# Kernel optimization log

Measured on AMD Instinct MI355X. Metric: run time of the kernel, lower is better.

## Reference

```python
import jax, jax.numpy as jnp
import numpy as np

E = 256
H = 8
DH = E // H
N = 200000
NEG = -1e9


def _normalize(x, eps=1e-12):
    # torch F.normalize: x / max(||x||_2, eps) along last dim
    n = jnp.linalg.norm(x, axis=-1, keepdims=True)
    return x / jnp.maximum(n, eps)


def setup_inputs() -> dict:
    key = jax.random.key(0)
    ks = jax.random.split(key, 16)
    s = 1.0 / np.sqrt(E)
    inp = {
        "context_vector": jax.random.normal(ks[0], (3 * E,), jnp.float32),
        "node_embeddings": jax.random.normal(ks[1], (N, E), jnp.float32),
        "invalid_action_mask": jax.random.randint(ks[2], (N,), 0, 2).astype(bool),
        # project_context: Linear(3E, E)
        "Wc": jax.random.normal(ks[3], (E, 3 * E), jnp.float32) * (1.0 / np.sqrt(3 * E)),
        "bc": jnp.zeros((E,), jnp.float32),
        # project_keys / project_values: Linear(E, E)
        "Wk": jax.random.normal(ks[4], (E, E), jnp.float32) * s,
        "bk": jnp.zeros((E,), jnp.float32),
        "Wv": jax.random.normal(ks[5], (E, E), jnp.float32) * s,
        "bv": jnp.zeros((E,), jnp.float32),
        # nn.MultiheadAttention packed in-projection and out-projection
        "in_proj_w": jax.random.normal(ks[6], (3 * E, E), jnp.float32) * s,
        "in_proj_b": jnp.zeros((3 * E,), jnp.float32),
        "out_proj_w": jax.random.normal(ks[7], (E, E), jnp.float32) * s,
        "out_proj_b": jnp.zeros((E,), jnp.float32),
        # project_attn_output: Linear(E, E)
        "Wo": jax.random.normal(ks[8], (E, E), jnp.float32) * s,
        "bo": jnp.zeros((E,), jnp.float32),
    }
    # guarantee at least one valid action
    inp["invalid_action_mask"] = inp["invalid_action_mask"].at[0].set(False)
    return inp


def reference(context_vector, node_embeddings, invalid_action_mask,
              Wc, bc, Wk, bk, Wv, bv,
              in_proj_w, in_proj_b, out_proj_w, out_proj_b, Wo, bo):
    valid = ~invalid_action_mask                        # [N]

    query = context_vector @ Wc.T + bc                  # [E]
    keys = _normalize(node_embeddings @ Wk.T + bk)      # [N, E]
    values = _normalize(node_embeddings @ Wv.T + bv)    # [N, E]

    # MultiheadAttention, single query, batch 1
    wq, wk2, wv2 = in_proj_w[:E], in_proj_w[E:2 * E], in_proj_w[2 * E:]
    bq, bk2, bv2 = in_proj_b[:E], in_proj_b[E:2 * E], in_proj_b[2 * E:]
    q = (query @ wq.T + bq).reshape(H, DH)              # [H, DH]
    k = (keys @ wk2.T + bk2).reshape(N, H, DH)          # [N, H, DH]
    v = (values @ wv2.T + bv2).reshape(N, H, DH)

    logits = jnp.einsum("hd,nhd->hn", q, k) / np.sqrt(DH)   # [H, N]
    logits = jnp.where(valid[None, :], logits, NEG)
    w = jax.nn.softmax(logits, axis=-1)                 # [H, N]
    attn = jnp.einsum("hn,nhd->hd", w, v).reshape(E)    # [E]
    attn = attn @ out_proj_w.T + out_proj_b             # [E]

    attn = _normalize(attn @ Wo.T + bo)                 # [E]

    # pointer scores over valid nodes (invalid -> prob 0)
    scores = jnp.where(valid, keys @ attn, NEG)         # [N]
    probs = jax.nn.softmax(scores)                      # [N]
    return probs
```

## Files before the change

### kernel.cpp

```cpp
#include <hip/hip_runtime.h>

#define NN 200000
#define NEGV -1000000000.0f

typedef __attribute__((ext_vector_type(8))) short bf16x8;
typedef __attribute__((ext_vector_type(4))) float f32x4;
typedef __attribute__((ext_vector_type(4))) unsigned int u32x4;

__device__ __forceinline__ float bf2f(unsigned short u){
  unsigned int x = ((unsigned int)u) << 16;
  return __builtin_bit_cast(float, x);
}
__device__ __forceinline__ unsigned short f2bf(float f){
  unsigned int x = __builtin_bit_cast(unsigned int, f);
  x += 0x7fffu + ((x >> 16) & 1u);
  return (unsigned short)(x >> 16);
}

static constexpr size_t OFF_RK     = 0;
static constexpr size_t OFF_RV     = 800256;
static constexpr size_t OFF_LOGITS = 1600512;
static constexpr size_t OFF_SCORES = 8000512;
static constexpr size_t OFF_QUERY  = 8800768;
static constexpr size_t OFF_Q2     = 8801792;
static constexpr size_t OFF_A2     = 8802816;
static constexpr size_t OFF_CONSTS = 8811008;
static constexpr size_t OFF_BIMG   = 8811264;
static constexpr size_t OFF_LSTAT  = 9081600;
static constexpr size_t OFF_MZ     = 9089792;
static constexpr size_t OFF_KATTN  = 9089856;
static constexpr size_t OFF_KB     = 9090880;
static constexpr size_t OFF_UPART  = 9090944;
static constexpr size_t OFF_TPART  = 13285248;
static constexpr size_t OFF_U      = 13301632;
static constexpr size_t OFF_T      = 13309824;
static constexpr size_t OFF_P3STAT = 13309888;
static constexpr size_t OFF_MZ3    = 13313984;
static constexpr size_t OFF_EMBBF  = 13314048;
static constexpr size_t WS_NEED_BF = OFF_EMBBF + (size_t)NN*512;

__global__ void k_conv(const float* __restrict__ emb, unsigned char* __restrict__ ebf){
  size_t stride = (size_t)gridDim.x * blockDim.x;
  for (size_t g = (size_t)blockIdx.x*blockDim.x + threadIdx.x; g < (size_t)NN*32; g += stride){
    const float* src = emb + g*8;
    float4 a = *(const float4*)src;
    float4 b = *(const float4*)(src + 4);
    u32x4 o;
    o.x = (unsigned int)f2bf(a.x) | ((unsigned int)f2bf(a.y) << 16);
    o.y = (unsigned int)f2bf(a.z) | ((unsigned int)f2bf(a.w) << 16);
    o.z = (unsigned int)f2bf(b.x) | ((unsigned int)f2bf(b.y) << 16);
    o.w = (unsigned int)f2bf(b.z) | ((unsigned int)f2bf(b.w) << 16);
    *(u32x4*)(ebf + g*16) = o;
  }
}

__global__ void k_prep1(const float* __restrict__ ctx, const float* __restrict__ Wc,
                        const float* __restrict__ bc, float* __restrict__ query){
  int tid = threadIdx.x, lane = tid & 63, wave = tid >> 6;
  float4 c0 = *(const float4*)(ctx + lane*4);
  float4 c1 = *(const float4*)(ctx + 256 + lane*4);
  float4 c2 = *(const float4*)(ctx + 512 + lane*4);
  #pragma unroll
  for (int rr = 0; rr < 2; rr++){
    int r = blockIdx.x*8 + wave*2 + rr;
    float4 w0 = *(const float4*)(Wc + (size_t)r*768 + lane*4);
    float4 w1 = *(const float4*)(Wc + (size_t)r*768 + 256 + lane*4);
    float4 w2 = *(const float4*)(Wc + (size_t)r*768 + 512 + lane*4);
    float d = w0.x*c0.x + w0.y*c0.y + w0.z*c0.z + w0.w*c0.w
            + w1.x*c1.x + w1.y*c1.y + w1.z*c1.z + w1.w*c1.w
            + w2.x*c2.x + w2.y*c2.y + w2.z*c2.z + w2.w*c2.w;
    #pragma unroll
    for (int m = 1; m < 64; m <<= 1) d += __shfl_xor(d, m);
    if (lane == 0) query[r] = d + bc[r];
  }
}

__global__ void k_prep2(const float* __restrict__ ipw, const float* __restrict__ ipb,
                        const float* __restrict__ query, float* __restrict__ q2){
  int tid = threadIdx.x, lane = tid & 63, wave = tid >> 6;
  float4 x4 = *(const float4*)(query + lane*4);
  #pragma unroll
  for (int rr = 0; rr < 2; rr++){
    int r = blockIdx.x*8 + wave*2 + rr;
    float4 w4 = *(const float4*)(ipw + (size_t)r*256 + lane*4);
    float d = w4.x*x4.x + w4.y*x4.y + w4.z*x4.z + w4.w*x4.w;
    #pragma unroll
    for (int m = 1; m < 64; m <<= 1) d += __shfl_xor(d, m);
    if (lane == 0) q2[r] = d + ipb[r];
  }
}

__global__ void k_prep3(const float* __restrict__ ipw, const float* __restrict__ ipb,
                        const float* __restrict__ q2, float* __restrict__ AH,
                        float* __restrict__ consts){
  int h = blockIdx.x, t = threadIdx.x;
  __shared__ float qs[32];
  if (t < 32) qs[t] = q2[h*32 + t];
  __syncthreads();
  float a = 0.f;
  #pragma unroll
  for (int d = 0; d < 32; d++) a += qs[d] * ipw[(size_t)(256 + h*32 + d)*256 + t];
  AH[h*256 + t] = a;
  if (t == 0){
    float ck = 0.f;
    for (int d = 0; d < 32; d++) ck += qs[d] * ipb[256 + h*32 + d];
    consts[8 + h] = ck;
  }
}

__global__ void k_prep4(const float* __restrict__ Wk, const float* __restrict__ AH,
                        float* __restrict__ A2p){
  int b = blockIdx.x, h = b >> 3, seg = b & 7, t = threadIdx.x;
  __shared__ float as[32];
  if (t < 32) as[t] = AH[h*256 + seg*32 + t];
  __syncthreads();
  float acc = 0.f;
  #pragma unroll
  for (int i = 0; i < 32; i++) acc += as[i] * Wk[(size_t)(seg*32 + i)*256 + t];
  A2p[(size_t)b*256 + t] = acc;
}

__global__ void k_prep5(const float* __restrict__ A2p, const float* __restrict__ AH,
                        const float* __restrict__ bk, float* __restrict__ A2,
                        float* __restrict__ consts){
  int h = blockIdx.x, t = threadIdx.x, lane = t & 63, wave = t >> 6;
  float s = 0.f;
  #pragma unroll
  for (int seg = 0; seg < 8; seg++) s += A2p[(size_t)(h*8 + seg)*256 + t];
  A2[h*256 + t] = s;
  float cc = AH[h*256 + t] * bk[t];
  #pragma unroll
  for (int m = 1; m < 64; m <<= 1) cc += __shfl_xor(cc, m);
  __shared__ float red[4];
  if (lane == 0) red[wave] = cc;
  __syncthreads();
  if (t == 0) consts[h] = red[0] + red[1] + red[2] + red[3];
}

__global__ void k_bimg(const float* __restrict__ Wk, const float* __restrict__ Wv,
                       const float* __restrict__ A2, unsigned char* __restrict__ bimg){
  int g = blockIdx.x*256 + threadIdx.x;
  if (g >= 8*528*4) return;
  int s = g / (528*4);
  int rem = g % (528*4);
  int col = rem >> 2, kg = rem & 3;
  int j0 = s*32 + kg*8;
  const float* src = nullptr;
  if (col < 256) src = Wk + col*256 + j0;
  else if (col < 512) src = Wv + (col-256)*256 + j0;
  else if (col < 520) src = A2 + (col-512)*256 + j0;
  unsigned short u[8];
  #pragma unroll
  for (int i = 0; i < 8; i++) u[i] = src ? f2bf(src[i]) : (unsigned short)0;
  uint4 o;
  o.x = (unsigned int)u[0] | ((unsigned int)u[1] << 16);
  o.y = (unsigned int)u[2] | ((unsigned int)u[3] << 16);
  o.z = (unsigned int)u[4] | ((unsigned int)u[5] << 16);
  o.w = (unsigned int)u[6] | ((unsigned int)u[7] << 16);
  unsigned int addr = (unsigned int)((col*64 + kg*16) ^ ((col & 7) << 4));
  *(uint4*)(bimg + (size_t)s*33792 + addr) = o;
}

template<int BF>
__launch_bounds__(256)
__global__ void k_main(const float* __restrict__ emb, const unsigned char* __restrict__ ebf,
                       const unsigned char* __restrict__ bimg,
                       const int* __restrict__ mask, const float* __restrict__ consts,
                       float* __restrict__ rk_g, float* __restrict__ rv_g,
                       float* __restrict__ logits){
  __shared__ float part[4][2][16];
  __shared__ float rkbuf[32];
  const int tid = threadIdx.x;
  const int lane = tid & 63, ch = tid >> 6;
  const int c = lane & 15, kg = lane >> 4;
  const int nb0 = blockIdx.x * 32;
  const unsigned bOff = (unsigned)((c*64 + kg*16) ^ ((c & 7) << 4));

  f32x4 acc[2][9];
  #pragma unroll
  for (int st = 0; st < 2; st++)
    #pragma unroll
    for (int f = 0; f < 9; f++) acc[st][f] = (f32x4){0.f, 0.f, 0.f, 0.f};

  if (BF){
    const unsigned char* aB0 = ebf + (size_t)(nb0 + c)*512 + kg*16;
    const unsigned char* aB1 = ebf + (size_t)(nb0 + 16 + c)*512 + kg*16;
    bf16x8 pa0[8], pa1[8];
    pa0[0] = *(const bf16x8*)(aB0);
    pa1[0] = *(const bf16x8*)(aB1);
    pa0[1] = *(const bf16x8*)(aB0 + 64);
    pa1[1] = *(const bf16x8*)(aB1 + 64);
    #pragma unroll
    for (int s = 0; s < 8; s++){
      if (s < 6){
        pa0[s+2] = *(const bf16x8*)(aB0 + (s+2)*64);
        pa1[s+2] = *(const bf16x8*)(aB1 + (s+2)*64);
      }
      const unsigned char* bs = bimg + (size_t)s*33792 + bOff;
      #pragma unroll
      for (int f = 0; f < 9; f++){
        const int cf = (f < 8) ? (ch*8 + f) : 32;
        bf16x8 bfv = *(const bf16x8*)(bs + (size_t)cf*1024);
        acc[0][f] = __builtin_amdgcn_mfma_f32_16x16x32_bf16(pa0[s], bfv, acc[0][f], 0, 0, 0);
        acc[1][f] = __builtin_amdgcn_mfma_f32_16x16x32_bf16(pa1[s], bfv, acc[1][f], 0, 0, 0);
      }
    }
  } else {
    #pragma unroll 2
    for (int s = 0; s < 8; s++){
      const float* a0p = emb + (size_t)(nb0 + c)*256 + s*32 + kg*8;
      const float* a1p = emb + (size_t)(nb0 + 16 + c)*256 + s*32 + kg*8;
      float4 x0 = *(const float4*)a0p, x1 = *(const float4*)(a0p + 4);
      float4 y0 = *(const float4*)a1p, y1 = *(const float4*)(a1p + 4);
      u32x4 u0, u1;
      u0.x = (unsigned int)f2bf(x0.x) | ((unsigned int)f2bf(x0.y) << 16);
      u0.y = (unsigned int)f2bf(x0.z) | ((unsigned int)f2bf(x0.w) << 16);
      u0.z = (unsigned int)f2bf(x1.x) | ((unsigned int)f2bf(x1.y) << 16);
      u0.w = (unsigned int)f2bf(x1.z) | ((unsigned int)f2bf(x1.w) << 16);
      u1.x = (unsigned int)f2bf(y0.x) | ((unsigned int)f2bf(y0.y) << 16);
      u1.y = (unsigned int)f2bf(y0.z) | ((unsigned int)f2bf(y0.w) << 16);
      u1.z = (unsigned int)f2bf(y1.x) | ((unsigned int)f2bf(y1.y) << 16);
      u1.w = (unsigned int)f2bf(y1.z) | ((unsigned int)f2bf(y1.w) << 16);
      bf16x8 af0 = __builtin_bit_cast(bf16x8, u0);
      bf16x8 af1 = __builtin_bit_cast(bf16x8, u1);
      const unsigned char* bs = bimg + (size_t)s*33792 + bOff;
      #pragma unroll
      for (int f = 0; f < 9; f++){
        const int cf = (f < 8) ? (ch*8 + f) : 32;
        bf16x8 bfv = *(const bf16x8*)(bs + (size_t)cf*1024);
        acc[0][f] = __builtin_amdgcn_mfma_f32_16x16x32_bf16(af0, bfv, acc[0][f], 0, 0, 0);
        acc[1][f] = __builtin_amdgcn_mfma_f32_16x16x32_bf16(af1, bfv, acc[1][f], 0, 0, 0);
      }
    }
  }

  #pragma unroll
  for (int st = 0; st < 2; st++){
    #pragma unroll
    for (int i = 0; i < 4; i++){
      float pp = 0.f;
      #pragma unroll
      for (int f = 0; f < 8; f++) pp += acc[st][f][i]*acc[st][f][i];
      #pragma unroll
      for (int m = 1; m < 16; m <<= 1) pp += __shfl_xor(pp, m);
      if (c == 0) part[ch][st][kg*4 + i] = pp;
    }
  }
  __syncthreads();
  if (tid < 32){
    int gs = tid >> 4, r = tid & 15;
    float rk = fmaxf(sqrtf(part[0][gs][r] + part[1][gs][r]), 1e-12f);
    float rv = fmaxf(sqrtf(part[2][gs][r] + part[3][gs][r]), 1e-12f);
    rk_g[nb0 + tid] = rk; rv_g[nb0 + tid] = rv;
    rkbuf[tid] = rk;
  }
  __syncthreads();
  if (ch == 3 && c < 8){
    const float rs32 = 0.17677669529663688f;
    float cb = consts[c], ck = consts[8 + c];
    #pragma unroll
    for (int st = 0; st < 2; st++){
      #pragma unroll
      for (int i = 0; i < 4; i++){
        int nl = st*16 + kg*4 + i;
        int n = nb0 + nl;
        float lg = (mask[n] == 0) ? ((acc[st][8][i] + cb)*rs32/rkbuf[nl] + ck*rs32) : NEGV;
        logits[(size_t)n*8 + c] = lg;
      }
    }
  }
}

__global__ void k_lstats(const float* __restrict__ logits, float* __restrict__ lstat){
  int tid = threadIdx.x;
  float m[8], z[8];
  #pragma unroll
  for (int h = 0; h < 8; h++){ m[h] = -3.0e38f; z[h] = 0.f; }
  for (int n = blockIdx.x*256 + tid; n < NN; n += 128*256){
    float4 a = *(const float4*)(logits + (size_t)n*8);
    float4 b = *(const float4*)(logits + (size_t)n*8 + 4);
    float l[8] = {a.x,a.y,a.z,a.w,b.x,b.y,b.z,b.w};
    #pragma unroll
    for (int h = 0; h < 8; h++){
      float M = fmaxf(m[h], l[h]);
      z[h] = z[h]*expf(m[h]-M) + expf(l[h]-M);
      m[h] = M;
    }
  }
  #pragma unroll
  for (int s = 1; s < 64; s <<= 1){
    #pragma unroll
    for (int h = 0; h < 8; h++){
      float m2 = __shfl_xor(m[h], s), z2 = __shfl_xor(z[h], s);
      float M = fmaxf(m[h], m2);
      z[h] = z[h]*expf(m[h]-M) + z2*expf(m2-M);
      m[h] = M;
    }
  }
  __shared__ float sm[4][8], sz[4][8];
  int wave = tid >> 6, lane = tid & 63;
  if (lane == 0){
    #pragma unroll
    for (int h = 0; h < 8; h++){ sm[wave][h] = m[h]; sz[wave][h] = z[h]; }
  }
  __syncthreads();
  if (tid < 8){
    float M = sm[0][tid], Z = sz[0][tid];
    #pragma unroll
    for (int w = 1; w < 4; w++){
      float M2 = fmaxf(M, sm[w][tid]);
      Z = Z*expf(M-M2) + sz[w][tid]*expf(sm[w][tid]-M2);
      M = M2;
    }
    lstat[(blockIdx.x*8 + tid)*2] = M;
    lstat[(blockIdx.x*8 + tid)*2 + 1] = Z;
  }
}

__global__ void k_mz(const float* __restrict__ lstat, float* __restrict__ MZ){
  int t = threadIdx.x;
  int h = t >> 3, seg = t & 7;
  float m = -3.0e38f, z = 0.f;
  for (int k = 0; k < 16; k++){
    int b = seg*16 + k;
    float m2 = lstat[(b*8 + h)*2], z2 = lstat[(b*8 + h)*2 + 1];
    float M = fmaxf(m, m2); z = z*expf(m-M) + z2*expf(m2-M); m = M;
  }
  #pragma unroll
  for (int s = 1; s < 8; s <<= 1){
    float m2 = __shfl_xor(m, s), z2 = __shfl_xor(z, s);
    float M = fmaxf(m, m2); z = z*expf(m-M) + z2*expf(m2-M); m = M;
  }
  if (seg == 0){ MZ[h] = m; MZ[8+h] = z; }
}

template<int BF>
__launch_bounds__(256)
__global__ void k_wsum(const void* __restrict__ embsrc, const float* __restrict__ logits,
                       const float* __restrict__ rv_g, const float* __restrict__ MZ,
                       float* __restrict__ upart, float* __restrict__ tpart){
  int tid = threadIdx.x, lane = tid & 63, wave = tid >> 6;
  int hl = lane & 31, h2 = lane >> 5;
  int gw = blockIdx.x*4 + wave;
  float Mh = MZ[hl & 7];
  float ua[8][8];
  #pragma unroll
  for (int h = 0; h < 8; h++)
    #pragma unroll
    for (int j = 0; j < 8; j++) ua[h][j] = 0.f;
  float tacc = 0.f;
  for (int p = gw; p < NN/2; p += 2048){
    int n = 2*p + h2;
    float e[8];
    if (BF){
      uint4 g = *(const uint4*)((const unsigned char*)embsrc + (size_t)n*512 + hl*16);
      e[0]=bf2f((unsigned short)(g.x&0xffff)); e[1]=bf2f((unsigned short)(g.x>>16));
      e[2]=bf2f((unsigned short)(g.y&0xffff)); e[3]=bf2f((unsigned short)(g.y>>16));
      e[4]=bf2f((unsigned short)(g.z&0xffff)); e[5]=bf2f((unsigned short)(g.z>>16));
      e[6]=bf2f((unsigned short)(g.w&0xffff)); e[7]=bf2f((unsigned short)(g.w>>16));
    } else {
      const float* ep = (const float*)embsrc + (size_t)n*256 + hl*8;
      float4 a = *(const float4*)ep, b = *(const float4*)(ep + 4);
      e[0]=a.x; e[1]=a.y; e[2]=a.z; e[3]=a.w; e[4]=b.x; e[5]=b.y; e[6]=b.z; e[7]=b.w;
    }
    float coef = 0.f;
    if (hl < 8) coef = expf(logits[(size_t)n*8 + hl] - Mh) / rv_g[n];
    tacc += coef;
    #pragma unroll
    for (int h = 0; h < 8; h++){
      float ch = __shfl(coef, h, 32);
      #pragma unroll
      for (int j = 0; j < 8; j++) ua[h][j] += ch * e[j];
    }
  }
  #pragma unroll
  for (int h = 0; h < 8; h++)
    #pragma unroll
    for (int j = 0; j < 8; j++) ua[h][j] += __shfl_xor(ua[h][j], 32);
  tacc += __shfl_xor(tacc, 32);
  __shared__ float ub[4][8][256];
  __shared__ float tb[4][8];
  if (h2 == 0){
    #pragma unroll
    for (int h = 0; h < 8; h++)
      #pragma unroll
      for (int j = 0; j < 8; j++) ub[wave][h][hl*8 + j] = ua[h][j];
    if (hl < 8) tb[wave][hl] = tacc;
  }
  __syncthreads();
  #pragma unroll
  for (int rep = 0; rep < 8; rep++){
    int idx = rep*256 + tid;
    int h = idx >> 8, j = idx & 255;
    upart[(size_t)blockIdx.x*2048 + h*256 + j] = ub[0][h][j]+ub[1][h][j]+ub[2][h][j]+ub[3][h][j];
  }
  if (tid < 8) tpart[blockIdx.x*8 + tid] = tb[0][tid]+tb[1][tid]+tb[2][tid]+tb[3][tid];
}

__global__ void k_ured(const float* __restrict__ upart, const float* __restrict__ tpart,
                       float* __restrict__ U, float* __restrict__ T){
  int b = blockIdx.x; int h = b >> 3, js = b & 7;
  int t = threadIdx.x; int j = js*32 + (t & 31); int br = t >> 5;
  float s = 0.f;
  for (int k = 0; k < 64; k++){
    int bb = k*8 + br;
    s += upart[(size_t)bb*2048 + h*256 + j];
  }
  __shared__ float sb[8][32];
  sb[br][t & 31] = s;
  __syncthreads();
  if (t < 32){
    float tot = 0.f;
    #pragma unroll
    for (int r = 0; r < 8; r++) tot += sb[r][t];
    U[h*256 + js*32 + t] = tot;
  }
  if (js == 0){
    float tp = 0.f;
    for (int i = t; i < 512; i += 256) tp += tpart[i*8 + h];
    #pragma unroll
    for (int m = 1; m < 64; m <<= 1) tp += __shfl_xor(tp, m);
    __shared__ float rr[4];
    if ((t & 63) == 0) rr[t >> 6] = tp;
    __syncthreads();
    if (t == 0) T[h] = rr[0]+rr[1]+rr[2]+rr[3];
  }
}

__global__ void k_att1(const float* __restrict__ U, const float* __restrict__ T,
                       const float* __restrict__ MZ, const float* __restrict__ Wv,
                       const float* __restrict__ bv, float* __restrict__ sh2g){
  int tid = threadIdx.x, lane = tid & 63, wave = tid >> 6;
  float4 uh[8];
  #pragma unroll
  for (int h = 0; h < 8; h++) uh[h] = *(const float4*)(U + h*256 + lane*4);
  #pragma unroll
  for (int rr = 0; rr < 2; rr++){
    int r = blockIdx.x*8 + wave*2 + rr;
    float4 w4 = *(const float4*)(Wv + (size_t)r*256 + lane*4);
    float acc[8];
    #pragma unroll
    for (int h = 0; h < 8; h++)
      acc[h] = w4.x*uh[h].x + w4.y*uh[h].y + w4.z*uh[h].z + w4.w*uh[h].w;
    #pragma unroll
    for (int m = 1; m < 64; m <<= 1)
      #pragma unroll
      for (int h = 0; h < 8; h++) acc[h] += __shfl_xor(acc[h], m);
    if (lane == 0){
      float bvr = bv[r];
      #pragma unroll
      for (int h = 0; h < 8; h++) sh2g[h*256 + r] = (acc[h] + bvr*T[h]) / MZ[8+h];
    }
  }
}

__global__ void k_att2(const float* __restrict__ ipw, const float* __restrict__ ipb,
                       const float* __restrict__ sh2g, float* __restrict__ a1g){
  int tid = threadIdx.x, lane = tid & 63, wave = tid >> 6;
  #pragma unroll
  for (int rr = 0; rr < 2; rr++){
    int r = blockIdx.x*8 + wave*2 + rr;
    int h = r >> 5;
    float4 x4 = *(const float4*)(sh2g + h*256 + lane*4);
    float4 w4 = *(const float4*)(ipw + (size_t)(512 + r)*256 + lane*4);
    float d = w4.x*x4.x + w4.y*x4.y + w4.z*x4.z + w4.w*x4.w;
    #pragma unroll
    for (int m = 1; m < 64; m <<= 1) d += __shfl_xor(d, m);
    if (lane == 0) a1g[r] = d + ipb[512 + r];
  }
}

__global__ void k_matvec(const float* __restrict__ W, const float* __restrict__ b,
                         const float* __restrict__ x, float* __restrict__ y){
  int tid = threadIdx.x, lane = tid & 63, wave = tid >> 6;
  float4 x4 = *(const float4*)(x + lane*4);
  #pragma unroll
  for (int rr = 0; rr < 2; rr++){
    int r = blockIdx.x*8 + wave*2 + rr;
    float4 w4 = *(const float4*)(W + (size_t)r*256 + lane*4);
    float d = w4.x*x4.x + w4.y*x4.y + w4.z*x4.z + w4.w*x4.w;
    #pragma unroll
    for (int m = 1; m < 64; m <<= 1) d += __shfl_xor(d, m);
    if (lane == 0) y[r] = d + b[r];
  }
}

__global__ void k_att5(const float* __restrict__ Wk, const float* __restrict__ o2g,
                       float* __restrict__ kp){
  int b = blockIdx.x, t = threadIdx.x;
  __shared__ float os[32];
  if (t < 32) os[t] = o2g[b*32 + t];
  __syncthreads();
  float acc = 0.f;
  #pragma unroll
  for (int i = 0; i < 32; i++) acc += os[i] * Wk[(size_t)(b*32 + i)*256 + t];
  kp[b*256 + t] = acc;
}

__global__ void k_fin(const float* __restrict__ o2g, const float* __restrict__ kp,
                      const float* __restrict__ bk, float* __restrict__ kattn,
                      float* __restrict__ kbout){
  int t = threadIdx.x, lane = t & 63, wave = t >> 6;
  __shared__ float red[4], red2[4];
  float o2v = o2g[t];
  float sq = o2v*o2v;
  #pragma unroll
  for (int m = 1; m < 64; m <<= 1) sq += __shfl_xor(sq, m);
  if (lane == 0) red[wave] = sq;
  float cb = o2v * bk[t];
  #pragma unroll
  for (int m = 1; m < 64; m <<= 1) cb += __shfl_xor(cb, m);
  if (lane == 0) red2[wave] = cb;
  __syncthreads();
  float nrm = fmaxf(sqrtf(red[0]+red[1]+red[2]+red[3]), 1e-12f);
  float s = 0.f;
  #pragma unroll
  for (int b = 0; b < 8; b++) s += kp[b*256 + t];
  kattn[t] = s / nrm;
  if (t == 0) kbout[0] = (red2[0]+red2[1]+red2[2]+red2[3]) / nrm;
}

template<int BF>
__launch_bounds__(256)
__global__ void k_scores(const void* __restrict__ embsrc, const float* __restrict__ rk_g,
                         const int* __restrict__ mask, const float* __restrict__ kattn,
                         const float* __restrict__ kbp, float* __restrict__ scores,
                         float* __restrict__ p3stat){
  int tid = threadIdx.x, lane = tid & 63, wave = tid >> 6;
  int hl = lane & 31, h2 = lane >> 5;
  __shared__ float ka[256];
  ka[tid] = kattn[tid];
  __syncthreads();
  float kb = kbp[0];
  float kv[8];
  #pragma unroll
  for (int j = 0; j < 8; j++) kv[j] = ka[hl*8 + j];
  int gw = blockIdx.x*4 + wave;
  float m = -3.0e38f, z = 0.f;
  for (int p = gw; p < NN/2; p += 2048){
    int n = 2*p + h2;
    float d;
    if (BF){
      uint4 g = *(const uint4*)((const unsigned char*)embsrc + (size_t)n*512 + hl*16);
      d  = bf2f((unsigned short)(g.x&0xffff))*kv[0] + bf2f((unsigned short)(g.x>>16))*kv[1];
      d += bf2f((unsigned short)(g.y&0xffff))*kv[2] + bf2f((unsigned short)(g.y>>16))*kv[3];
      d += bf2f((unsigned short)(g.z&0xffff))*kv[4] + bf2f((unsigned short)(g.z>>16))*kv[5];
      d += bf2f((unsigned short)(g.w&0xffff))*kv[6] + bf2f((unsigned short)(g.w>>16))*kv[7];
    } else {
      const float* ep = (const float*)embsrc + (size_t)n*256 + hl*8;
      float4 a = *(const float4*)ep, b = *(const float4*)(ep + 4);
      d = a.x*kv[0]+a.y*kv[1]+a.z*kv[2]+a.w*kv[3]+b.x*kv[4]+b.y*kv[5]+b.z*kv[6]+b.w*kv[7];
    }
    #pragma unroll
    for (int s = 1; s < 32; s <<= 1) d += __shfl_xor(d, s);
    if (hl == 0){
      float sc = (mask[n] == 0) ? ((d + kb) / rk_g[n]) : NEGV;
      scores[n] = sc;
      float M = fmaxf(m, sc);
      z = z*expf(m - M) + expf(sc - M);
      m = M;
    }
  }
  float m2 = __shfl_xor(m, 32), z2 = __shfl_xor(z, 32);
  float M = fmaxf(m, m2); z = z*expf(m-M) + z2*expf(m2-M); m = M;
  __shared__ float rm[4], rz[4];
  if (lane == 0){ rm[wave] = m; rz[wave] = z; }
  __syncthreads();
  if (tid == 0){
    float Mx = rm[0], Z = rz[0];
    for (int w = 1; w < 4; w++){
      float M2 = fmaxf(Mx, rm[w]);
      Z = Z*expf(Mx - M2) + rz[w]*expf(rm[w] - M2);
      Mx = M2;
    }
    p3stat[blockIdx.x*2] = Mx; p3stat[blockIdx.x*2+1] = Z;
  }
}

__global__ void k_mz3(const float* __restrict__ p3stat, float* __restrict__ MZ3){
  int t = threadIdx.x;
  float m = p3stat[t*2], z = p3stat[t*2+1];
  {
    float m2 = p3stat[(t+256)*2], z2 = p3stat[(t+256)*2+1];
    float M = fmaxf(m, m2); z = z*expf(m-M) + z2*expf(m2-M); m = M;
  }
  #pragma unroll
  for (int mm = 1; mm < 64; mm <<= 1){
    float ms = __shfl_xor(m, mm), zs = __shfl_xor(z, mm);
    float Mx = fmaxf(m, ms); z = z*expf(m-Mx) + zs*expf(ms-Mx); m = Mx;
  }
  __shared__ float rm[4], rz[4];
  if ((t&63)==0){ rm[t>>6]=m; rz[t>>6]=z; }
  __syncthreads();
  if (t==0){
    float M=rm[0], Z=rz[0];
    for (int w=1; w<4; w++){ float Mx=fmaxf(M,rm[w]); Z=Z*expf(M-Mx)+rz[w]*expf(rm[w]-Mx); M=Mx; }
    MZ3[0]=M; MZ3[1]=Z;
  }
}

__global__ void k_probs(const float* __restrict__ scores, const float* __restrict__ MZ3,
                        float* __restrict__ out){
  float M = MZ3[0], iZ = 1.0f / MZ3[1];
  for (int n = blockIdx.x*256 + threadIdx.x; n < NN; n += 512*256)
    out[n] = expf(scores[n] - M) * iZ;
}

extern "C" void kernel_launch(void* const* d_in, const int* in_sizes, int n_in,
                              void* d_out, int out_size, void* d_ws, size_t ws_size,
                              hipStream_t stream){
  (void)in_sizes; (void)n_in; (void)out_size;
  const float* ctx = (const float*)d_in[0];
  const float* emb = (const float*)d_in[1];
  const int*   mask= (const int*)d_in[2];
  const float* Wc  = (const float*)d_in[3];
  const float* bc  = (const float*)d_in[4];
  const float* Wk  = (const float*)d_in[5];
  const float* bk  = (const float*)d_in[6];
  const float* Wv  = (const float*)d_in[7];
  const float* bv  = (const float*)d_in[8];
  const float* ipw = (const float*)d_in[9];
  const float* ipb = (const float*)d_in[10];
  const float* opw = (const float*)d_in[11];
  const float* opb = (const float*)d_in[12];
  const float* Wo  = (const float*)d_in[13];
  const float* bo  = (const float*)d_in[14];
  float* out = (float*)d_out;
  char* ws = (char*)d_ws;

  float* rk     = (float*)(ws + OFF_RK);
  float* rv     = (float*)(ws + OFF_RV);
  float* logits = (float*)(ws + OFF_LOGITS);
  float* scores = (float*)(ws + OFF_SCORES);
  float* query  = (float*)(ws + OFF_QUERY);
  float* q2     = (float*)(ws + OFF_Q2);
  float* A2     = (float*)(ws + OFF_A2);
  float* consts = (float*)(ws + OFF_CONSTS);
  unsigned char* bimg = (unsigned char*)(ws + OFF_BIMG);
  float* lstat  = (float*)(ws + OFF_LSTAT);
  float* MZ     = (float*)(ws + OFF_MZ);
  float* kattn  = (float*)(ws + OFF_KATTN);
  float* kb     = (float*)(ws + OFF_KB);
  float* upart  = (float*)(ws + OFF_UPART);
  float* tpart  = (float*)(ws + OFF_TPART);
  float* U      = (float*)(ws + OFF_U);
  float* T      = (float*)(ws + OFF_T);
  float* p3stat = (float*)(ws + OFF_P3STAT);
  float* MZ3    = (float*)(ws + OFF_MZ3);
  float* AH   = (float*)(ws + OFF_UPART + 32768);
  float* A2p  = (float*)(ws + OFF_UPART + 65536);
  float* sh2g = (float*)(ws + OFF_UPART + 0);
  float* a1g  = (float*)(ws + OFF_UPART + 8192);
  float* o1g  = (float*)(ws + OFF_UPART + 9216);
  float* o2g  = (float*)(ws + OFF_UPART + 10240);
  float* kp   = (float*)(ws + OFF_UPART + 11264);

  const bool bf = ws_size >= WS_NEED_BF;
  unsigned char* ebf = bf ? (unsigned char*)(ws + OFF_EMBBF) : nullptr;

  if (bf) k_conv<<<2048, 256, 0, stream>>>(emb, ebf);
  k_prep1 <<<32,  256, 0, stream>>>(ctx, Wc, bc, query);
  k_prep2 <<<32,  256, 0, stream>>>(ipw, ipb, query, q2);
  k_prep3 <<<8,   256, 0, stream>>>(ipw, ipb, q2, AH, consts);
  k_prep4 <<<64,  256, 0, stream>>>(Wk, AH, A2p);
  k_prep5 <<<8,   256, 0, stream>>>(A2p, AH, bk, A2, consts);
  k_bimg  <<<66,  256, 0, stream>>>(Wk, Wv, A2, bimg);
  if (bf) k_main<1><<<6250, 256, 0, stream>>>(emb, ebf, bimg, mask, consts, rk, rv, logits);
  else    k_main<0><<<6250, 256, 0, stream>>>(emb, nullptr, bimg, mask, consts, rk, rv, logits);
  k_lstats<<<128, 256, 0, stream>>>(logits, lstat);
  k_mz    <<<1,   64,  0, stream>>>(lstat, MZ);
  if (bf) k_wsum<1><<<512, 256, 0, stream>>>(ebf, logits, rv, MZ, upart, tpart);
  else    k_wsum<0><<<512, 256, 0, stream>>>(emb, logits, rv, MZ, upart, tpart);
  k_ured  <<<64,  256, 0, stream>>>(upart, tpart, U, T);
  k_att1  <<<32,  256, 0, stream>>>(U, T, MZ, Wv, bv, sh2g);
  k_att2  <<<32,  256, 0, stream>>>(ipw, ipb, sh2g, a1g);
  k_matvec<<<32,  256, 0, stream>>>(opw, opb, a1g, o1g);
  k_matvec<<<32,  256, 0, stream>>>(Wo, bo, o1g, o2g);
  k_att5  <<<8,   256, 0, stream>>>(Wk, o2g, kp);
  k_fin   <<<1,   256, 0, stream>>>(o2g, kp, bk, kattn, kb);
  if (bf) k_scores<1><<<512, 256, 0, stream>>>(ebf, rk, mask, kattn, kb, scores, p3stat);
  else    k_scores<0><<<512, 256, 0, stream>>>(emb, rk, mask, kattn, kb, scores, p3stat);
  k_mz3   <<<1,   256, 0, stream>>>(p3stat, MZ3);
  k_probs <<<512, 256, 0, stream>>>(scores, MZ3, out);
}
```

Baseline: 324.7 us.

## Make main projection kernel persistent with weight fragments staged in LDS

Replaces the 6250-block main projection kernel with a 256-block persistent kernel whose blocks each load their share of the bf16 weight image into 136KB of LDS once, then loop over node tiles. Blocks are split into key-norm and value-norm halves, each wave computing 17 fragments (16 columns plus the logit column) per 32-node tile. The aim is to drop the repeated global/L2 weight reads and per-block launch overhead. In exchange each wave holds 34 accumulators, occupancy is limited to one block per CU, and the embedding tiles are read twice, once by each half.

Result: slower. 456.0 us (+40.5%).

```diff
diff --git a/kernel.cpp b/kernel.cpp
--- a/kernel.cpp
+++ b/kernel.cpp
@@ -161,13 +161,93 @@
   *(uint4*)(bimg + (size_t)s*33792 + addr) = o;
 }
 
-template<int BF>
+__launch_bounds__(256, 1)
+__global__ void k_mainp(const unsigned char* __restrict__ ebf,
+                        const unsigned char* __restrict__ bimg,
+                        const int* __restrict__ mask, const float* __restrict__ consts,
+                        float* __restrict__ rk_g, float* __restrict__ rv_g,
+                        float* __restrict__ logits){
+  extern __shared__ unsigned char smB[];
+  const int tid = threadIdx.x;
+  const int lane = tid & 63, wave = tid >> 6;
+  const int c = lane & 15, kg = lane >> 4;
+  const bool isK = (blockIdx.x < 128);
+  const int bid = isK ? blockIdx.x : (blockIdx.x - 128);
+  const int F0 = isK ? 0 : 16;
+  const unsigned bOff = (unsigned)((c*64 + kg*16) ^ ((c & 7) << 4));
+  float* nrm = isK ? rk_g : rv_g;
+
+  #pragma unroll
+  for (int it = 0; it < 34; it++){
+    int chunk = it*4 + wave;
+    int s = chunk / 17, fi = chunk % 17;
+    int frag = (fi == 16) ? 32 : (F0 + fi);
+    *(uint4*)&smB[(size_t)chunk*1024 + lane*16] =
+        *(const uint4*)(bimg + (size_t)s*33792 + (size_t)frag*1024 + lane*16);
+  }
+  __syncthreads();
+
+  float cb = 0.f, ck = 0.f;
+  if (c < 8){ cb = consts[c]; ck = consts[8 + c]; }
+  const float rs32 = 0.17677669529663688f;
+  const int gw = bid*4 + wave;
+
+  for (int p = gw; p < NN/32; p += 512){
+    const unsigned char* base = ebf + (size_t)p*16384 + (size_t)c*512 + kg*16;
+    bf16x8 a0[8], a1[8];
+    #pragma unroll
+    for (int s = 0; s < 8; s++){
+      a0[s] = *(const bf16x8*)(base + s*64);
+      a1[s] = *(const bf16x8*)(base + 8192 + s*64);
+    }
+    f32x4 acc0[17], acc1[17];
+    {
+      const unsigned char* bs = smB;
+      #pragma unroll
+      for (int fi = 0; fi < 17; fi++){
+        bf16x8 bfv = *(const bf16x8*)(bs + fi*1024 + bOff);
+        acc0[fi] = __builtin_amdgcn_mfma_f32_16x16x32_bf16(a0[0], bfv, (f32x4){0.f,0.f,0.f,0.f}, 0, 0, 0);
+        acc1[fi] = __builtin_amdgcn_mfma_f32_16x16x32_bf16(a1[0], bfv, (f32x4){0.f,0.f,0.f,0.f}, 0, 0, 0);
+      }
+    }
+    #pragma unroll
+    for (int s = 1; s < 8; s++){
+      const unsigned char* bs = smB + (size_t)s*17408;
+      #pragma unroll
+      for (int fi = 0; fi < 17; fi++){
+        bf16x8 bfv = *(const bf16x8*)(bs + fi*1024 + bOff);
+        acc0[fi] = __builtin_amdgcn_mfma_f32_16x16x32_bf16(a0[s], bfv, acc0[fi], 0, 0, 0);
+        acc1[fi] = __builtin_amdgcn_mfma_f32_16x16x32_bf16(a1[s], bfv, acc1[fi], 0, 0, 0);
+      }
+    }
+    auto epi = [&](f32x4 (&ac)[17], int nbase){
+      #pragma unroll
+      for (int i = 0; i < 4; i++){
+        float pp = 0.f;
+        #pragma unroll
+        for (int fi = 0; fi < 16; fi++) pp += ac[fi][i]*ac[fi][i];
+        #pragma unroll
+        for (int m = 1; m < 16; m <<= 1) pp += __shfl_xor(pp, m);
+        float r = fmaxf(sqrtf(pp), 1e-12f);
+        int n = nbase + kg*4 + i;
+        if (c == i) nrm[n] = r;
+        if (isK && c < 8){
+          float lg = (mask[n] == 0) ? ((ac[16][i] + cb)*rs32/r + ck*rs32) : NEGV;
+          logits[(size_t)n*8 + c] = lg;
+        }
+      }
+    };
+    int nb = p*32;
+    epi(acc0, nb);
+    epi(acc1, nb + 16);
+  }
+}
+
 __launch_bounds__(256)
-__global__ void k_main(const float* __restrict__ emb, const unsigned char* __restrict__ ebf,
-                       const unsigned char* __restrict__ bimg,
-                       const int* __restrict__ mask, const float* __restrict__ consts,
-                       float* __restrict__ rk_g, float* __restrict__ rv_g,
-                       float* __restrict__ logits){
+__global__ void k_main0(const float* __restrict__ emb, const unsigned char* __restrict__ bimg,
+                        const int* __restrict__ mask, const float* __restrict__ consts,
+                        float* __restrict__ rk_g, float* __restrict__ rv_g,
+                        float* __restrict__ logits){
   __shared__ float part[4][2][16];
   __shared__ float rkbuf[32];
   const int tid = threadIdx.x;
@@ -182,55 +262,30 @@
     #pragma unroll
     for (int f = 0; f < 9; f++) acc[st][f] = (f32x4){0.f, 0.f, 0.f, 0.f};
 
-  if (BF){
-    const unsigned char* aB0 = ebf + (size_t)(nb0 + c)*512 + kg*16;
-    const unsigned char* aB1 = ebf + (size_t)(nb0 + 16 + c)*512 + kg*16;
-    bf16x8 pa0[8], pa1[8];
-    pa0[0] = *(const bf16x8*)(aB0);
-    pa1[0] = *(const bf16x8*)(aB1);
-    pa0[1] = *(const bf16x8*)(aB0 + 64);
-    pa1[1] = *(const bf16x8*)(aB1 + 64);
-    #pragma unroll
-    for (int s = 0; s < 8; s++){
-      if (s < 6){
-        pa0[s+2] = *(const bf16x8*)(aB0 + (s+2)*64);
-        pa1[s+2] = *(const bf16x8*)(aB1 + (s+2)*64);
-      }
-      const unsigned char* bs = bimg + (size_t)s*33792 + bOff;
-      #pragma unroll
-      for (int f = 0; f < 9; f++){
-        const int cf = (f < 8) ? (ch*8 + f) : 32;
-        bf16x8 bfv = *(const bf16x8*)(bs + (size_t)cf*1024);
-        acc[0][f] = __builtin_amdgcn_mfma_f32_16x16x32_bf16(pa0[s], bfv, acc[0][f], 0, 0, 0);
-        acc[1][f] = __builtin_amdgcn_mfma_f32_16x16x32_bf16(pa1[s], bfv, acc[1][f], 0, 0, 0);
-      }
-    }
-  } else {
-    #pragma unroll 2
-    for (int s = 0; s < 8; s++){
-      const float* a0p = emb + (size_t)(nb0 + c)*256 + s*32 + kg*8;
-      const float* a1p = emb + (size_t)(nb0 + 16 + c)*256 + s*32 + kg*8;
-      float4 x0 = *(const float4*)a0p, x1 = *(const float4*)(a0p + 4);
-      float4 y0 = *(const float4*)a1p, y1 = *(const float4*)(a1p + 4);
-      u32x4 u0, u1;
-      u0.x = (unsigned int)f2bf(x0.x) | ((unsigned int)f2bf(x0.y) << 16);
-      u0.y = (unsigned int)f2bf(x0.z) | ((unsigned int)f2bf(x0.w) << 16);
-      u0.z = (unsigned int)f2bf(x1.x) | ((unsigned int)f2bf(x1.y) << 16);
-      u0.w = (unsigned int)f2bf(x1.z) | ((unsigned int)f2bf(x1.w) << 16);
-      u1.x = (unsigned int)f2bf(y0.x) | ((unsigned int)f2bf(y0.y) << 16);
-      u1.y = (unsigned int)f2bf(y0.z) | ((unsigned int)f2bf(y0.w) << 16);
-      u1.z = (unsigned int)f2bf(y1.x) | ((unsigned int)f2bf(y1.y) << 16);
-      u1.w = (unsigned int)f2bf(y1.z) | ((unsigned int)f2bf(y1.w) << 16);
-      bf16x8 af0 = __builtin_bit_cast(bf16x8, u0);
-      bf16x8 af1 = __builtin_bit_cast(bf16x8, u1);
-      const unsigned char* bs = bimg + (size_t)s*33792 + bOff;
-      #pragma unroll
-      for (int f = 0; f < 9; f++){
-        const int cf = (f < 8) ? (ch*8 + f) : 32;
-        bf16x8 bfv = *(const bf16x8*)(bs + (size_t)cf*1024);
-        acc[0][f] = __builtin_amdgcn_mfma_f32_16x16x32_bf16(af0, bfv, acc[0][f], 0, 0, 0);
-        acc[1][f] = __builtin_amdgcn_mfma_f32_16x16x32_bf16(af1, bfv, acc[1][f], 0, 0, 0);
-      }
+  #pragma unroll 2
+  for (int s = 0; s < 8; s++){
+    const float* a0p = emb + (size_t)(nb0 + c)*256 + s*32 + kg*8;
+    const float* a1p = emb + (size_t)(nb0 + 16 + c)*256 + s*32 + kg*8;
+    float4 x0 = *(const float4*)a0p, x1 = *(const float4*)(a0p + 4);
+    float4 y0 = *(const float4*)a1p, y1 = *(const float4*)(a1p + 4);
+    u32x4 u0, u1;
+    u0.x = (unsigned int)f2bf(x0.x) | ((unsigned int)f2bf(x0.y) << 16);
+    u0.y = (unsigned int)f2bf(x0.z) | ((unsigned int)f2bf(x0.w) << 16);
+    u0.z = (unsigned int)f2bf(x1.x) | ((unsigned int)f2bf(x1.y) << 16);
+    u0.w = (unsigned int)f2bf(x1.z) | ((unsigned int)f2bf(x1.w) << 16);
+    u1.x = (unsigned int)f2bf(y0.x) | ((unsigned int)f2bf(y0.y) << 16);
+    u1.y = (unsigned int)f2bf(y0.z) | ((unsigned int)f2bf(y0.w) << 16);
+    u1.z = (unsigned int)f2bf(y1.x) | ((unsigned int)f2bf(y1.y) << 16);
+    u1.w = (unsigned int)f2bf(y1.z) | ((unsigned int)f2bf(y1.w) << 16);
+    bf16x8 af0 = __builtin_bit_cast(bf16x8, u0);
+    bf16x8 af1 = __builtin_bit_cast(bf16x8, u1);
+    const unsigned char* bs = bimg + (size_t)s*33792 + bOff;
+    #pragma unroll
+    for (int f = 0; f < 9; f++){
+      const int cf = (f < 8) ? (ch*8 + f) : 32;
+      bf16x8 bfv = *(const bf16x8*)(bs + (size_t)cf*1024);
+      acc[0][f] = __builtin_amdgcn_mfma_f32_16x16x32_bf16(af0, bfv, acc[0][f], 0, 0, 0);
+      acc[1][f] = __builtin_amdgcn_mfma_f32_16x16x32_bf16(af1, bfv, acc[1][f], 0, 0, 0);
     }
   }
 
@@ -665,8 +720,8 @@
   k_prep4 <<<64,  256, 0, stream>>>(Wk, AH, A2p);
   k_prep5 <<<8,   256, 0, stream>>>(A2p, AH, bk, A2, consts);
   k_bimg  <<<66,  256, 0, stream>>>(Wk, Wv, A2, bimg);
-  if (bf) k_main<1><<<6250, 256, 0, stream>>>(emb, ebf, bimg, mask, consts, rk, rv, logits);
-  else    k_main<0><<<6250, 256, 0, stream>>>(emb, nullptr, bimg, mask, consts, rk, rv, logits);
+  if (bf) k_mainp<<<256, 256, 139264, stream>>>(ebf, bimg, mask, consts, rk, rv, logits);
+  else    k_main0<<<6250, 256, 0, stream>>>(emb, bimg, mask, consts, rk, rv, logits);
   k_lstats<<<128, 256, 0, stream>>>(logits, lstat);
   k_mz    <<<1,   64,  0, stream>>>(lstat, MZ);
   if (bf) k_wsum<1><<<512, 256, 0, stream>>>(ebf, logits, rv, MZ, upart, tpart);
```
